# Optimization experiments

Measured on AMD Instinct MI355X. Metric: run time of the kernel, lower is better.

Reference implementation:

```python
import jax, jax.numpy as jnp
import numpy as np
from jax import lax

NEIGHBORS = 3


def _dwconv(x, w, b, dil):
    # depthwise Conv3d, kernel (9,3,3), temporal pad 4, spatial dilation `dil`
    out = lax.conv_general_dilated(
        x, w, window_strides=(1, 1, 1),
        padding=[(4, 4), (dil, dil), (dil, dil)],
        rhs_dilation=(1, dil, dil),
        dimension_numbers=('NCDHW', 'OIDHW', 'NCDHW'),
        feature_group_count=w.shape[0])
    return out + b[None, :, None, None, None]


def setup_inputs() -> dict:
    key = jax.random.key(0)
    ks = jax.random.split(key, 20)
    N, C, T, H, W = 2, 512, 96, 14, 14
    rc = C // 16
    nrm = lambda k, shape: (jax.random.normal(k, shape, jnp.float32) * 0.02)
    inp = {
        'x': jax.random.normal(ks[0], (N, C, T, H, W), jnp.float32),
        'down_conv2_w': nrm(ks[1], (C, C)),
        'down_conv_w': nrm(ks[2], (rc, C)),
        'conv_back_w': nrm(ks[3], (C, rc)),
        'weights2': jnp.ones((2 * NEIGHBORS,), jnp.float32) / (2 * NEIGHBORS),
        'weights4': jnp.ones((3,), jnp.float32) / 3,
        'weights': jnp.ones((3,), jnp.float32) / 3,
        'query': jax.random.uniform(ks[4], (1, 1, C), jnp.float32),
        'q_w': nrm(ks[5], (C, C)), 'q_b': nrm(ks[6], (C,)),
        'k_w': nrm(ks[7], (C, C)), 'k_b': nrm(ks[8], (C,)),
        'v_w': nrm(ks[9], (C, C)), 'v_b': nrm(ks[10], (C,)),
        'c_w': nrm(ks[11], (C, C)), 'c_b': nrm(ks[12], (C,)),
        'sa1_w': nrm(ks[13], (rc, 1, 9, 3, 3)), 'sa1_b': nrm(ks[14], (rc,)),
        'sa2_w': nrm(ks[15], (rc, 1, 9, 3, 3)), 'sa2_b': nrm(ks[16], (rc,)),
        'sa3_w': nrm(ks[17], (rc, 1, 9, 3, 3)), 'sa3_b': nrm(ks[18], (rc,)),
    }
    return inp


def reference(x, down_conv2_w, down_conv_w, conv_back_w, weights2, weights4, weights,
              query, q_w, q_b, k_w, k_b, v_w, v_b, c_w, c_b,
              sa1_w, sa1_b, sa2_w, sa2_b, sa3_w, sa3_b):
    N, C, T, H, W = x.shape
    nb = NEIGHBORS
    win = 2 * nb + 1

    # --- AttentionPool2d: single head, single learned query token ---
    kv = x.reshape(N, C, T, H * W).transpose(3, 0, 2, 1).reshape(H * W, N * T, C)  # (L,B,C)
    q = jnp.broadcast_to(query, (1, N * T, C))
    qp = (q @ q_w.T + q_b) * (C ** -0.5)          # head_dim == C since num_heads=1
    kp = kv @ k_w.T + k_b
    vp = kv @ v_w.T + v_b
    attn = jax.nn.softmax(jnp.einsum('pbc,lbc->bpl', qp, kp), axis=-1)  # (B,1,L)
    att_out = jnp.einsum('bpl,lbc->pbc', attn, vp) @ c_w.T + c_b        # (1,B,C)
    x_att = att_out.reshape(1, N, T, C).transpose(1, 3, 2, 0)           # (N,C,T,1)

    # --- pooled queries ---
    x_mean = jnp.mean(x, axis=(3, 4))[..., None]   # (N,C,T,1)
    x_max = jnp.max(x, axis=(3, 4))[..., None]     # (N,C,T,1)
    xq = x_mean * weights4[0] + x_max * weights4[1] + x_att * weights4[2]

    # --- 1x1 conv + temporal unfold (window 7, zero pad 3), drop center frame ---
    x2 = jnp.einsum('oc,ncthw->nothw', down_conv2_w, x)
    xp = jnp.pad(x2, ((0, 0), (0, 0), (nb, nb), (0, 0), (0, 0)))
    windows = jnp.stack([xp[:, :, i:i + T] for i in range(win)], axis=3)  # (N,C,T,7,H,W)
    idx = np.array([i for i in range(win) if i != nb])                    # exclude center
    upfold = windows[:, :, :, idx] * weights2[None, None, None, :, None, None]
    upfold = upfold.reshape(N, C, T, 2 * nb * H * W)                      # (N,C,T,L)

    # --- local correlation / clustering with sigmoid-0.5 gating ---
    aff = jnp.einsum('nctp,nctl->ntpl', xq, upfold)                       # (N,T,1,L)
    feat = jnp.einsum('nctl,ntpl->nctp', upfold, jax.nn.sigmoid(aff) - 0.5)  # (N,C,T,1)
    features = feat[..., None]                                            # (N,C,T,1,1)

    # --- multi-branch dilated depthwise conv fusion ---
    x_down = jnp.einsum('oc,ncthw->nothw', down_conv_w, x)                # (N,rc,T,H,W)
    agg = (_dwconv(x_down, sa1_w, sa1_b, 1) * weights[0]
           + _dwconv(x_down, sa2_w, sa2_b, 2) * weights[1]
           + _dwconv(x_down, sa3_w, sa3_b, 3) * weights[2])
    agg = jnp.einsum('oc,ncthw->nothw', conv_back_w, agg)                 # (N,C,T,H,W)

    return features * (jax.nn.sigmoid(agg) - 0.5)
```

## Files before the change

### kernel.cpp

```cpp
#include <hip/hip_runtime.h>
#include <hip/hip_bf16.h>

using bf16 = __hip_bfloat16;
typedef __attribute__((ext_vector_type(4))) unsigned short ushort4v;

#define N_  2
#define C_  512
#define T_  96
#define H_  14
#define W_  14
#define HW_ 196
#define RC_ 32
#define B_  (N_*T_)
#define SC_ (T_*HW_)
#define XTOT (N_*C_*T_*HW_)

#define VQB   0
#define VKB   512
#define VVB   1024
#define VCB   1536
#define VQRY  2048
#define VSAB  2560
#define VW2   2688
#define VW4   2696
#define VWTS  2700
#define VECS_TOTAL 2720

__device__ __forceinline__ float b2f(bf16 v){ return __bfloat162float(v); }
__device__ __forceinline__ float u2f(unsigned short u){ return __uint_as_float(((unsigned)u)<<16); }
__device__ __forceinline__ float sigm(float x){ return 1.f/(1.f+__expf(-x)); }
__device__ __forceinline__ unsigned short f2bu(float f){
    bf16 b = __float2bfloat16(f);
    return *(unsigned short*)&b;
}

__device__ __forceinline__ float ldd(const void* p, size_t i, bool f32){
    if (f32) return ((const float*)p)[i];
    else     return b2f(((const bf16*)p)[i]);
}

__global__ void probe_kernel(const void* __restrict__ x, int* __restrict__ flag){
    if (blockIdx.x==0 && threadIdx.x==0){
        const unsigned short* h = (const unsigned short*)x;
        int wild = 0;
        for (int i=0;i<128;i++){
            int e = (h[i] >> 7) & 0xFF;
            if (e < 100 || e > 150) wild++;
        }
        flag[0] = (wild > 16) ? 1 : 0;
    }
}

__global__ void prep_w2t_kernel(const void* __restrict__ dcw2, float* __restrict__ w2t,
                                const int* __restrict__ flag){
    bool f32 = flag[0]!=0;
    int i = blockIdx.x*256 + threadIdx.x;
    if (i < C_*C_){
        int in = i / C_, out = i % C_;
        w2t[i] = ldd(dcw2, (size_t)out*C_ + in, f32);
    }
}

#define PM_OLD (16384+16384+7776+512*5+96+6+3+3)
#define PM_TOTAL (PM_OLD + 262144 + 262144)
__global__ void prep_misc_kernel(const void* dcw, const void* cbw,
                                 const void* sa1w, const void* sa2w, const void* sa3w,
                                 const void* q_b, const void* k_b, const void* v_b,
                                 const void* c_b, const void* query,
                                 const void* sa1b, const void* sa2b, const void* sa3b,
                                 const void* w2, const void* w4, const void* wts,
                                 const void* v_w, const void* c_w,
                                 float* __restrict__ dwt, float* __restrict__ cbwf,
                                 float* __restrict__ saw, float* __restrict__ vecs,
                                 float* __restrict__ vwt, float* __restrict__ cwt,
                                 const int* __restrict__ flag){
    bool f32 = flag[0]!=0;
    int i = blockIdx.x*256 + threadIdx.x;
    if (i >= PM_TOTAL) return;
    if (i < 16384){ dwt[i] = ldd(dcw, i, f32); return; }
    i -= 16384;
    if (i < 16384){ cbwf[i] = ldd(cbw, i, f32); return; }
    i -= 16384;
    if (i < 7776){
        const void* s = (i<2592)? sa1w : ((i<5184)? sa2w : sa3w);
        int j = (i<2592)? i : ((i<5184)? i-2592 : i-5184);
        saw[i] = ldd(s, j, f32); return;
    }
    i -= 7776;
    if (i < 512){ vecs[VQB +i] = ldd(q_b,  i, f32); return; } i -= 512;
    if (i < 512){ vecs[VKB +i] = ldd(k_b,  i, f32); return; } i -= 512;
    if (i < 512){ vecs[VVB +i] = ldd(v_b,  i, f32); return; } i -= 512;
    if (i < 512){ vecs[VCB +i] = ldd(c_b,  i, f32); return; } i -= 512;
    if (i < 512){ vecs[VQRY+i] = ldd(query,i, f32); return; } i -= 512;
    if (i < 96){
        const void* s = (i<32)? sa1b : ((i<64)? sa2b : sa3b);
        vecs[VSAB+i] = ldd(s, i&31, f32); return;
    }
    i -= 96;
    if (i < 6){ vecs[VW2+i] = ldd(w2, i, f32); return; } i -= 6;
    if (i < 3){ vecs[VW4+i] = ldd(w4, i, f32); return; } i -= 3;
    if (i < 3){ vecs[VWTS+i] = ldd(wts, i, f32); return; } i -= 3;
    if (i < 262144){ int r=i/C_, c=i%C_; vwt[i] = ldd(v_w, (size_t)c*C_+r, f32); return; }
    i -= 262144;
    { int r=i/C_, c=i%C_; cwt[i] = ldd(c_w, (size_t)c*C_+r, f32); }
}

#define TCH 128
__global__ void __launch_bounds__(256) cvt_tr_kernel(const void* __restrict__ x,
                                                     bf16* __restrict__ xt,
                                                     const int* __restrict__ flag){
    bool f32 = flag[0]!=0;
    int bt = blockIdx.x;
    int n = bt / T_, t = bt % T_;
    int c0 = blockIdx.y * TCH;
    __shared__ bf16 tile[TCH*197];
    int tid = threadIdx.x;
    const size_t ibase = (((size_t)n*C_ + c0)*T_ + t)*HW_;
    for (int i=tid; i<TCH*49; i+=256){
        int cr = i / 49, l4 = (i - cr*49)*4;
        size_t gi = ibase + (size_t)cr*SC_ + l4;
        bf16* dp = &tile[cr*197 + l4];
        if (f32){
            float4 v = *(const float4*)((const float*)x + gi);
            dp[0]=__float2bfloat16(v.x); dp[1]=__float2bfloat16(v.y);
            dp[2]=__float2bfloat16(v.z); dp[3]=__float2bfloat16(v.w);
        } else {
            ushort4v u = *(const ushort4v*)((const bf16*)x + gi);
            #pragma unroll
            for (int k=0;k<4;k++) *(unsigned short*)&dp[k] = u[k];
        }
    }
    __syncthreads();
    bf16* obase = xt + (size_t)bt*HW_*C_ + c0;
    for (int i=tid; i<HW_*TCH/4; i+=256){
        int l = i >> 5, cg = (i & 31)*4;
        ushort4v u;
        #pragma unroll
        for (int k=0;k<4;k++) u[k] = *(unsigned short*)&tile[(cg+k)*197 + l];
        *(ushort4v*)(obase + (size_t)l*C_ + cg) = u;
    }
}

__global__ void __launch_bounds__(64) qproj1_kernel(const void* __restrict__ q_w,
        const float* __restrict__ vecs, float* __restrict__ qp,
        const int* __restrict__ flag){
    bool f32 = flag[0]!=0;
    int c = blockIdx.x;
    int lane = threadIdx.x;
    float acc = 0.f;
    #pragma unroll
    for (int i=lane;i<C_;i+=64)
        acc += vecs[VQRY+i] * ldd(q_w, (size_t)c*C_+i, f32);
    #pragma unroll
    for (int off=32; off>0; off>>=1) acc += __shfl_down(acc, off);
    if (lane==0) qp[c] = (acc + vecs[VQB+c]) * 0.044194173824159216f;
}

__global__ void __launch_bounds__(256) qproj2_kernel(const void* __restrict__ k_w,
        const float* __restrict__ vecs, const float* __restrict__ qp,
        float* __restrict__ qk_out, const int* __restrict__ flag){
    bool f32 = flag[0]!=0;
    __shared__ float sh[256];
    int tid = threadIdx.x;
    if (blockIdx.x < 8){
        int c = blockIdx.x*64 + (tid&63);
        int isub = tid>>6;
        float acc = 0.f;
        for (int i=isub*128; i<isub*128+128; i++)
            acc += qp[i] * ldd(k_w, (size_t)i*C_ + c, f32);
        sh[tid] = acc;
        __syncthreads();
        if (tid < 64)
            qk_out[c] = sh[tid] + sh[tid+64] + sh[tid+128] + sh[tid+192];
    } else {
        float acc = 0.f;
        for (int i=tid;i<C_;i+=256) acc += qp[i]*vecs[VKB+i];
        sh[tid] = acc;
        __syncthreads();
        if (tid==0){
            float d=0.f;
            for (int i=0;i<256;i++) d += sh[i];
            qk_out[C_] = d;
        }
    }
}

__global__ void __launch_bounds__(512) f1_kernel(const bf16* __restrict__ xt,
        const float* __restrict__ qk, const float* __restrict__ vecs,
        float* __restrict__ pooled, float* __restrict__ mm){
    int b = blockIdx.x;
    __shared__ float sm[HW_];
    __shared__ float red[2];
    __shared__ float r8[8][C_];
    int tid = threadIdx.x, wave = tid>>6, lane = tid&63;
    float qkr[8];
    #pragma unroll
    for (int k=0;k<4;k++){ qkr[k] = qk[lane*4+k]; qkr[4+k] = qk[256+lane*4+k]; }
    float qkC = qk[C_];
    const bf16* fbase = xt + (size_t)b*HW_*C_;
    for (int l=wave; l<HW_; l+=8){
        const bf16* row = fbase + (size_t)l*C_;
        ushort4v u1 = *(const ushort4v*)(row + lane*4);
        ushort4v u2 = *(const ushort4v*)(row + 256 + lane*4);
        float a = 0.f;
        #pragma unroll
        for (int k=0;k<4;k++) a += qkr[k]*u2f(u1[k]) + qkr[4+k]*u2f(u2[k]);
        #pragma unroll
        for (int off=32; off>0; off>>=1) a += __shfl_down(a, off);
        if (lane==0) sm[l] = a + qkC;
    }
    __syncthreads();
    if (tid < 64){
        float m = -1e30f;
        for (int l=tid; l<HW_; l+=64) m = fmaxf(m, sm[l]);
        #pragma unroll
        for (int off=32; off>0; off>>=1) m = fmaxf(m, __shfl_down(m, off));
        if (tid==0) red[0] = m;
    }
    __syncthreads();
    if (tid < HW_) sm[tid] = __expf(sm[tid]-red[0]);
    __syncthreads();
    if (tid < 64){
        float s = 0.f;
        for (int l=tid; l<HW_; l+=64) s += sm[l];
        #pragma unroll
        for (int off=32; off>0; off>>=1) s += __shfl_down(s, off);
        if (tid==0) red[1] = 1.f/s;
    }
    __syncthreads();
    if (tid < HW_) sm[tid] *= red[1];
    __syncthreads();
    float sa[8], pa[8], ma[8];
    #pragma unroll
    for (int k=0;k<8;k++){ sa[k]=0.f; pa[k]=0.f; ma[k]=-1e30f; }
    for (int l=wave; l<HW_; l+=8){
        const bf16* row = fbase + (size_t)l*C_;
        ushort4v u1 = *(const ushort4v*)(row + lane*4);
        ushort4v u2 = *(const ushort4v*)(row + 256 + lane*4);
        float smv = sm[l];
        #pragma unroll
        for (int k=0;k<4;k++){
            float v1 = u2f(u1[k]), v2 = u2f(u2[k]);
            sa[k]   += v1; ma[k]   = fmaxf(ma[k],  v1); pa[k]   += smv*v1;
            sa[4+k] += v2; ma[4+k] = fmaxf(ma[4+k],v2); pa[4+k] += smv*v2;
        }
    }
    int c1 = lane*4, c2 = 256+lane*4;
    #pragma unroll
    for (int k=0;k<4;k++){ r8[wave][c1+k]=pa[k]; r8[wave][c2+k]=pa[4+k]; }
    __syncthreads();
    int c = tid;
    float pltot = 0.f;
    #pragma unroll
    for (int w=0;w<8;w++) pltot += r8[w][c];
    __syncthreads();
    #pragma unroll
    for (int k=0;k<4;k++){ r8[wave][c1+k]=sa[k]; r8[wave][c2+k]=sa[4+k]; }
    __syncthreads();
    float stot = 0.f;
    #pragma unroll
    for (int w=0;w<8;w++) stot += r8[w][c];
    __syncthreads();
    #pragma unroll
    for (int k=0;k<4;k++){ r8[wave][c1+k]=ma[k]; r8[wave][c2+k]=ma[4+k]; }
    __syncthreads();
    float mtot = -1e30f;
    #pragma unroll
    for (int w=0;w<8;w++) mtot = fmaxf(mtot, r8[w][c]);
    pooled[(size_t)b*C_+c] = pltot;
    float w40=vecs[VW4+0], w41=vecs[VW4+1];
    mm[(size_t)b*C_+c] = stot*(1.f/HW_)*w40 + mtot*w41;
}

__global__ void __launch_bounds__(512) proj_kernel(const float* __restrict__ pooled,
        const float* __restrict__ mm, const float* __restrict__ vwt,
        const float* __restrict__ cwt, const void* __restrict__ dcw2,
        const float* __restrict__ vecs, float* __restrict__ xq,
        float* __restrict__ yq, const int* __restrict__ flag){
    bool f32 = flag[0]!=0;
    int b = blockIdx.x, c = threadIdx.x;
    __shared__ float p_s[C_];
    __shared__ float pre_s[C_];
    __shared__ float xq_s[C_];
    p_s[c] = pooled[(size_t)b*C_ + c];
    __syncthreads();
    float pre = vecs[VVB+c];
    for (int i=0;i<C_;i++) pre += p_s[i]*vwt[(size_t)i*C_+c];
    pre_s[c] = pre;
    __syncthreads();
    float att = vecs[VCB+c];
    for (int i=0;i<C_;i++) att += pre_s[i]*cwt[(size_t)i*C_+c];
    float xqv = mm[(size_t)b*C_+c] + vecs[VW4+2]*att;
    xq[(size_t)b*C_+c] = xqv;
    xq_s[c] = xqv;
    __syncthreads();
    float yqv = 0.f;
    for (int i=0;i<C_;i++) yqv += xq_s[i]*ldd(dcw2, (size_t)i*C_+c, f32);
    yq[(size_t)b*C_+c] = yqv;
}

#define QROWS 49
#define B6C   (B_*6*C_)
__global__ void __launch_bounds__(512) corr2gz_kernel(const bf16* __restrict__ xt,
        const float* __restrict__ yq, const float* __restrict__ vecs,
        float* __restrict__ zpart){
    const int offs[6] = {-3,-2,-1,1,2,3};
    int frame = blockIdx.x;
    int qq = blockIdx.y;
    int n = frame / T_, tp = frame % T_;
    int l0 = qq*QROWS;
    __shared__ bf16 xs[QROWS*C_];
    __shared__ float a_s[6][QROWS];
    int tid = threadIdx.x, lane = tid&63, wave = tid>>6;
    const ushort4v* src = (const ushort4v*)(xt + ((size_t)frame*HW_ + l0)*C_);
    ushort4v* dst = (ushort4v*)xs;
    for (int i=tid; i<QROWS*C_/4; i+=512) dst[i] = src[i];
    bool val[6]; float w2r[6]; float yqr[6][8];
    #pragma unroll
    for (int jj=0;jj<6;jj++){
        int tt = tp - offs[jj];
        val[jj] = (tt>=0 && tt<T_);
        w2r[jj] = vecs[VW2+jj];
        if (val[jj]){
            const float* yb = yq + (size_t)(n*T_+tt)*C_;
            #pragma unroll
            for (int k=0;k<4;k++){ yqr[jj][k]=yb[lane*4+k]; yqr[jj][4+k]=yb[256+lane*4+k]; }
        } else {
            #pragma unroll
            for (int k=0;k<8;k++) yqr[jj][k]=0.f;
        }
    }
    __syncthreads();
    for (int li=wave; li<QROWS; li+=8){
        ushort4v u1 = *(const ushort4v*)(xs + li*C_ + lane*4);
        ushort4v u2 = *(const ushort4v*)(xs + li*C_ + 256 + lane*4);
        float xf[8];
        #pragma unroll
        for (int k=0;k<4;k++){ xf[k]=u2f(u1[k]); xf[4+k]=u2f(u2[k]); }
        float a[6];
        #pragma unroll
        for (int jj=0;jj<6;jj++){
            float s=0.f;
            #pragma unroll
            for (int k=0;k<8;k++) s += yqr[jj][k]*xf[k];
            a[jj]=s;
        }
        #pragma unroll
        for (int off=32; off>0; off>>=1){
            #pragma unroll
            for (int jj=0;jj<6;jj++) a[jj] += __shfl_down(a[jj], off);
        }
        if (lane==0){
            #pragma unroll
            for (int jj=0;jj<6;jj++)
                a_s[jj][li] = val[jj] ? w2r[jj]*(sigm(w2r[jj]*a[jj])-0.5f) : 0.f;
        }
    }
    __syncthreads();
    int e = tid;
    float acc[6] = {0.f,0.f,0.f,0.f,0.f,0.f};
    for (int li=0; li<QROWS; ++li){
        float xv = b2f(xs[li*C_ + e]);
        #pragma unroll
        for (int jj=0;jj<6;jj++) acc[jj] += a_s[jj][li]*xv;
    }
    #pragma unroll
    for (int jj=0;jj<6;jj++){
        if (val[jj]){
            int b = n*T_ + (tp - offs[jj]);
            zpart[(size_t)qq*B6C + ((size_t)b*6+jj)*C_ + e] = acc[jj];
        }
    }
}

__global__ void __launch_bounds__(128) corr2f_kernel(const float* __restrict__ zpart,
        const float* __restrict__ w2t, float* __restrict__ feat){
    const int offs[6] = {-3,-2,-1,1,2,3};
    int b = blockIdx.x, c0 = blockIdx.y*128;
    int t = b % T_;
    int tid = threadIdx.x;
    __shared__ float z_s[C_];
    for (int e=tid; e<C_; e+=128){
        float s = 0.f;
        #pragma unroll
        for (int jj=0;jj<6;jj++){
            int tj = t + offs[jj];
            if (tj<0 || tj>=T_) continue;
            const float* zp = zpart + ((size_t)b*6+jj)*C_ + e;
            s += zp[0] + zp[B6C] + zp[2*B6C] + zp[3*(size_t)B6C];
        }
        z_s[e] = s;
    }
    __syncthreads();
    int c = c0 + tid;
    float acc = 0.f;
    for (int e=0;e<C_;e++) acc += w2t[(size_t)e*C_+c]*z_s[e];
    feat[(size_t)b*C_+c] = acc;
}

#define XPAD 8
#define XROW (C_+XPAD)
__global__ void __launch_bounds__(256) xdown_kernel(const bf16* __restrict__ xt,
                                                    const float* __restrict__ dwt,
                                                    bf16* __restrict__ xd){
    int b = blockIdx.x, n=b/T_, t=b%T_;
    int l0 = blockIdx.y*8;
    int nl = HW_ - l0; if (nl > 8) nl = 8;
    __shared__ bf16 xs[8*XROW];
    int tid = threadIdx.x;
    const bf16* fbase = xt + (size_t)b*HW_*C_ + (size_t)l0*C_;
    for (int i=tid; i<nl*(C_/4); i+=256){
        int row = i >> 7, gc = (i & 127)*4;
        *(ushort4v*)(xs + row*XROW + gc) = *(const ushort4v*)(fbase + (size_t)row*C_ + gc);
    }
    __syncthreads();
    int r = tid>>3, ls = tid&7;
    if (ls < nl){
        float acc = 0.f;
        const bf16* xr = xs + ls*XROW;
        const float* wr = dwt + (size_t)r*C_;
        #pragma unroll 4
        for (int c4=0; c4<C_; c4+=4){
            ushort4v u = *(const ushort4v*)(xr + c4);
            float4 w = *(const float4*)(wr + c4);
            acc += w.x*u2f(u[0]) + w.y*u2f(u[1])
                 + w.z*u2f(u[2]) + w.w*u2f(u[3]);
        }
        xd[(((size_t)n*RC_+r)*T_ + t)*HW_ + l0 + ls] = __float2bfloat16(acc);
    }
}

#define TPAD 21
#define TROW 20
#define TFRM (TROW*TPAD)
__global__ void __launch_bounds__(256) dwconv_kernel(const bf16* __restrict__ xd,
        const float* __restrict__ saw, const float* __restrict__ vecs,
        float* __restrict__ aggs){
    int nr = blockIdx.x;
    int t  = blockIdx.y;
    int r  = nr % RC_;
    __shared__ float tile[9*TFRM];
    __shared__ float wsm[3][81];
    int tid = threadIdx.x;
    for (int i=tid;i<9*TFRM;i+=256) tile[i] = 0.f;
    if (tid < 81){
        wsm[0][tid]=saw[       r*81+tid];
        wsm[1][tid]=saw[2592 + r*81+tid];
        wsm[2][tid]=saw[5184 + r*81+tid];
    }
    __syncthreads();
    const bf16* base = xd + (size_t)nr*T_*HW_;
    for (int i=tid;i<9*HW_;i+=256){
        int kt = i/HW_, hw = i - kt*HW_;
        int tg = t - 4 + kt;
        if (tg>=0 && tg<T_){
            int h = hw/W_, w = hw - h*W_;
            tile[kt*TFRM + (h+3)*TPAD + (w+3)] = b2f(base[(size_t)tg*HW_ + hw]);
        }
    }
    __syncthreads();
    if (tid < HW_){
        int h = tid/W_, w = tid - h*W_;
        float w0=vecs[VWTS+0], w1=vecs[VWTS+1], w2v=vecs[VWTS+2];
        float cbias = w0*vecs[VSAB+r] + w1*vecs[VSAB+32+r] + w2v*vecs[VSAB+64+r];
        float bacc[3];
        #pragma unroll
        for (int br=0;br<3;br++){
            int d = br+1;
            float s = 0.f;
            #pragma unroll
            for (int kt=0;kt<9;kt++){
                const float* tb = &tile[kt*TFRM + (h+3-d)*TPAD + (w+3-d)];
                const float* wp = &wsm[br][kt*9];
                s += wp[0]*tb[0]          + wp[1]*tb[d]          + wp[2]*tb[2*d]
                   + wp[3]*tb[d*TPAD]     + wp[4]*tb[d*TPAD+d]   + wp[5]*tb[d*TPAD+2*d]
                   + wp[6]*tb[2*d*TPAD]   + wp[7]*tb[2*d*TPAD+d] + wp[8]*tb[2*d*TPAD+2*d];
            }
            bacc[br] = s;
        }
        float acc = cbias + w0*bacc[0] + w1*bacc[1] + w2v*bacc[2];
        aggs[(size_t)nr*T_*HW_ + (size_t)t*HW_ + tid] = acc;
    }
}

__global__ void __launch_bounds__(256) final_kernel(const float* __restrict__ aggs,
                                                    const float* __restrict__ cbwf,
                                                    const float* __restrict__ feat,
                                                    float* __restrict__ out){
    int b = blockIdx.x, n = b/T_, t = b%T_;
    int c0 = blockIdx.y*128;
    int hw = threadIdx.x;
    if (hw >= HW_) return;
    float ra[RC_];
    #pragma unroll
    for (int r=0;r<RC_;r++)
        ra[r] = aggs[(((size_t)n*RC_+r)*T_ + t)*HW_ + hw];
    const float* fb = feat + (size_t)b*C_;
    for (int ci=0;ci<128;ci++){
        int c = c0+ci;
        const float* wr = cbwf + c*RC_;
        float a = 0.f;
        #pragma unroll
        for (int r=0;r<RC_;r++) a += wr[r]*ra[r];
        out[(((size_t)n*C_+c)*T_ + t)*HW_ + hw] = fb[c]*(sigm(a)-0.5f);
    }
}

extern "C" void kernel_launch(void* const* d_in, const int* in_sizes, int n_in,
                              void* d_out, int out_size, void* d_ws, size_t ws_size,
                              hipStream_t stream){
    const void* x      = d_in[0];
    const void* dcw2   = d_in[1];
    const void* dcw    = d_in[2];
    const void* cbw    = d_in[3];
    const void* w2     = d_in[4];
    const void* w4     = d_in[5];
    const void* wts    = d_in[6];
    const void* query  = d_in[7];
    const void* q_w    = d_in[8];
    const void* q_b    = d_in[9];
    const void* k_w    = d_in[10];
    const void* k_b    = d_in[11];
    const void* v_w    = d_in[12];
    const void* v_b    = d_in[13];
    const void* c_w    = d_in[14];
    const void* c_b    = d_in[15];
    const void* sa1w   = d_in[16];
    const void* sa1b   = d_in[17];
    const void* sa2w   = d_in[18];
    const void* sa2b   = d_in[19];
    const void* sa3w   = d_in[20];
    const void* sa3b   = d_in[21];
    float* out = (float*)d_out;

    float* ws    = (float*)d_ws;
    int*   flag  = (int*)ws;
    float* qk    = ws + 16;
    float* qp    = qk + 1024;
    float* pooled= qp + 1024;
    float* mm    = pooled + 98304;
    float* xq    = mm + 98304;
    float* yq    = xq + 98304;
    float* feat  = yq + 98304;
    float* w2t   = feat + 98304;
    float* vwt   = w2t + 262144;
    float* cwt   = vwt + 262144;
    float* dwt   = cwt + 262144;
    float* cbwf  = dwt + 16384;
    float* saw   = cbwf + 16384;
    float* vecs  = saw + 7936;
    float* aggs  = vecs + VECS_TOTAL;
    bf16*  xd    = (bf16*)(aggs + 1204224);
    bf16*  xt    = (bf16*)d_out;
    float* zpart = (float*)(xt + (size_t)XTOT);

    probe_kernel<<<1, 64, 0, stream>>>(x, flag);
    prep_w2t_kernel<<<(C_*C_+255)/256, 256, 0, stream>>>(dcw2, w2t, flag);
    prep_misc_kernel<<<(PM_TOTAL+255)/256, 256, 0, stream>>>(
        dcw, cbw, sa1w, sa2w, sa3w, q_b, k_b, v_b, c_b, query,
        sa1b, sa2b, sa3b, w2, w4, wts, v_w, c_w,
        dwt, cbwf, saw, vecs, vwt, cwt, flag);
    cvt_tr_kernel<<<dim3(B_, C_/TCH), 256, 0, stream>>>(x, xt, flag);

    qproj1_kernel<<<C_, 64, 0, stream>>>(q_w, vecs, qp, flag);
    qproj2_kernel<<<9, 256, 0, stream>>>(k_w, vecs, qp, qk, flag);
    f1_kernel<<<B_, 512, 0, stream>>>(xt, qk, vecs, pooled, mm);
    proj_kernel<<<B_, C_, 0, stream>>>(pooled, mm, vwt, cwt, dcw2, vecs, xq, yq, flag);

    corr2gz_kernel<<<dim3(B_, 4), 512, 0, stream>>>(xt, yq, vecs, zpart);
    corr2f_kernel<<<dim3(B_, 4), 128, 0, stream>>>(zpart, w2t, feat);

    xdown_kernel<<<dim3(B_, 25), 256, 0, stream>>>(xt, dwt, xd);
    dwconv_kernel<<<dim3(N_*RC_, T_), 256, 0, stream>>>(xd, saw, vecs, aggs);
    final_kernel<<<dim3(B_, 4), 256, 0, stream>>>(aggs, cbwf, feat, out);
}
```

Measured before the change: 647.1 us.

## Fuse channel down-projection into correlation kernel reusing its shared-memory tile

The separate xdown kernel, which re-read the whole bf16 transposed input from global memory, is removed. Its 512-to-32 channel projection is now computed inside corr2gz_kernel from the 49-row tile already staged in shared memory, with each wave producing four output channels. The shared tile rows are padded to 516 elements to reduce LDS bank conflicts on the row-strided reads. This saves one full pass over the input and one launch, but adds serial work to each correlation block, which could lengthen its critical path given the small grid of 768 blocks.

```diff
diff --git a/kernel.cpp b/kernel.cpp
--- a/kernel.cpp
+++ b/kernel.cpp
@@ -300,21 +300,25 @@
 }
 
 #define QROWS 49
+#define XR    516
 #define B6C   (B_*6*C_)
 __global__ void __launch_bounds__(512) corr2gz_kernel(const bf16* __restrict__ xt,
         const float* __restrict__ yq, const float* __restrict__ vecs,
-        float* __restrict__ zpart){
+        const float* __restrict__ dwt, float* __restrict__ zpart,
+        bf16* __restrict__ xd){
     const int offs[6] = {-3,-2,-1,1,2,3};
     int frame = blockIdx.x;
     int qq = blockIdx.y;
     int n = frame / T_, tp = frame % T_;
     int l0 = qq*QROWS;
-    __shared__ bf16 xs[QROWS*C_];
+    __shared__ bf16 xs[QROWS*XR];
     __shared__ float a_s[6][QROWS];
     int tid = threadIdx.x, lane = tid&63, wave = tid>>6;
     const ushort4v* src = (const ushort4v*)(xt + ((size_t)frame*HW_ + l0)*C_);
-    ushort4v* dst = (ushort4v*)xs;
-    for (int i=tid; i<QROWS*C_/4; i+=512) dst[i] = src[i];
+    for (int i=tid; i<QROWS*128; i+=512){
+        int row = i>>7, g4 = (i&127)*4;
+        *(ushort4v*)(xs + row*XR + g4) = src[i];
+    }
     bool val[6]; float w2r[6]; float yqr[6][8];
     #pragma unroll
     for (int jj=0;jj<6;jj++){
@@ -332,8 +336,8 @@
     }
     __syncthreads();
     for (int li=wave; li<QROWS; li+=8){
-        ushort4v u1 = *(const ushort4v*)(xs + li*C_ + lane*4);
-        ushort4v u2 = *(const ushort4v*)(xs + li*C_ + 256 + lane*4);
+        ushort4v u1 = *(const ushort4v*)(xs + li*XR + lane*4);
+        ushort4v u2 = *(const ushort4v*)(xs + li*XR + 256 + lane*4);
         float xf[8];
         #pragma unroll
         for (int k=0;k<4;k++){ xf[k]=u2f(u1[k]); xf[4+k]=u2f(u2[k]); }
@@ -357,18 +361,50 @@
         }
     }
     __syncthreads();
-    int e = tid;
-    float acc[6] = {0.f,0.f,0.f,0.f,0.f,0.f};
-    for (int li=0; li<QROWS; ++li){
-        float xv = b2f(xs[li*C_ + e]);
-        #pragma unroll
-        for (int jj=0;jj<6;jj++) acc[jj] += a_s[jj][li]*xv;
-    }
-    #pragma unroll
-    for (int jj=0;jj<6;jj++){
-        if (val[jj]){
-            int b = n*T_ + (tp - offs[jj]);
-            zpart[(size_t)qq*B6C + ((size_t)b*6+jj)*C_ + e] = acc[jj];
+    {
+        int e = tid;
+        float acc[6] = {0.f,0.f,0.f,0.f,0.f,0.f};
+        for (int li=0; li<QROWS; ++li){
+            float xv = b2f(xs[li*XR + e]);
+            #pragma unroll
+            for (int jj=0;jj<6;jj++) acc[jj] += a_s[jj][li]*xv;
+        }
+        #pragma unroll
+        for (int jj=0;jj<6;jj++){
+            if (val[jj]){
+                int b = n*T_ + (tp - offs[jj]);
+                zpart[(size_t)qq*B6C + ((size_t)b*6+jj)*C_ + e] = acc[jj];
+            }
+        }
+    }
+    {
+        int r0 = __builtin_amdgcn_readfirstlane(wave)*4;
+        if (lane < QROWS){
+            const bf16* xr = xs + lane*XR;
+            const float* w0 = dwt + (size_t)(r0+0)*C_;
+            const float* w1 = dwt + (size_t)(r0+1)*C_;
+            const float* w2p= dwt + (size_t)(r0+2)*C_;
+            const float* w3 = dwt + (size_t)(r0+3)*C_;
+            float a0=0.f, a1=0.f, a2=0.f, a3=0.f;
+            for (int c4=0; c4<C_; c4+=4){
+                ushort4v u = *(const ushort4v*)(xr + c4);
+                float x0=u2f(u[0]), x1=u2f(u[1]), x2=u2f(u[2]), x3=u2f(u[3]);
+                float4 wa = *(const float4*)(w0 + c4);
+                float4 wb = *(const float4*)(w1 + c4);
+                float4 wc = *(const float4*)(w2p+ c4);
+                float4 wd = *(const float4*)(w3 + c4);
+                a0 += wa.x*x0 + wa.y*x1 + wa.z*x2 + wa.w*x3;
+                a1 += wb.x*x0 + wb.y*x1 + wb.z*x2 + wb.w*x3;
+                a2 += wc.x*x0 + wc.y*x1 + wc.z*x2 + wc.w*x3;
+                a3 += wd.x*x0 + wd.y*x1 + wd.z*x2 + wd.w*x3;
+            }
+            int gl = l0 + lane;
+            size_t base = (((size_t)n*RC_ + r0)*T_ + tp)*HW_ + gl;
+            size_t step = (size_t)T_*HW_;
+            xd[base       ] = __float2bfloat16(a0);
+            xd[base+  step] = __float2bfloat16(a1);
+            xd[base+2*step] = __float2bfloat16(a2);
+            xd[base+3*step] = __float2bfloat16(a3);
         }
     }
 }
@@ -396,38 +432,6 @@
     float acc = 0.f;
     for (int e=0;e<C_;e++) acc += w2t[(size_t)e*C_+c]*z_s[e];
     feat[(size_t)b*C_+c] = acc;
-}
-
-#define XPAD 8
-#define XROW (C_+XPAD)
-__global__ void __launch_bounds__(256) xdown_kernel(const bf16* __restrict__ xt,
-                                                    const float* __restrict__ dwt,
-                                                    bf16* __restrict__ xd){
-    int b = blockIdx.x, n=b/T_, t=b%T_;
-    int l0 = blockIdx.y*8;
-    int nl = HW_ - l0; if (nl > 8) nl = 8;
-    __shared__ bf16 xs[8*XROW];
-    int tid = threadIdx.x;
-    const bf16* fbase = xt + (size_t)b*HW_*C_ + (size_t)l0*C_;
-    for (int i=tid; i<nl*(C_/4); i+=256){
-        int row = i >> 7, gc = (i & 127)*4;
-        *(ushort4v*)(xs + row*XROW + gc) = *(const ushort4v*)(fbase + (size_t)row*C_ + gc);
-    }
-    __syncthreads();
-    int r = tid>>3, ls = tid&7;
-    if (ls < nl){
-        float acc = 0.f;
-        const bf16* xr = xs + ls*XROW;
-        const float* wr = dwt + (size_t)r*C_;
-        #pragma unroll 4
-        for (int c4=0; c4<C_; c4+=4){
-            ushort4v u = *(const ushort4v*)(xr + c4);
-            float4 w = *(const float4*)(wr + c4);
-            acc += w.x*u2f(u[0]) + w.y*u2f(u[1])
-                 + w.z*u2f(u[2]) + w.w*u2f(u[3]);
-        }
-        xd[(((size_t)n*RC_+r)*T_ + t)*HW_ + l0 + ls] = __float2bfloat16(acc);
-    }
 }
 
 #define TPAD 21
@@ -567,10 +571,9 @@
     f1_kernel<<<B_, 512, 0, stream>>>(xt, qk, vecs, pooled, mm);
     proj_kernel<<<B_, C_, 0, stream>>>(pooled, mm, vwt, cwt, dcw2, vecs, xq, yq, flag);
 
-    corr2gz_kernel<<<dim3(B_, 4), 512, 0, stream>>>(xt, yq, vecs, zpart);
+    corr2gz_kernel<<<dim3(B_, 4), 512, 0, stream>>>(xt, yq, vecs, dwt, zpart, xd);
     corr2f_kernel<<<dim3(B_, 4), 128, 0, stream>>>(zpart, w2t, feat);
 
-    xdown_kernel<<<dim3(B_, 25), 256, 0, stream>>>(xt, dwt, xd);
     dwconv_kernel<<<dim3(N_*RC_, T_), 256, 0, stream>>>(xd, saw, vecs, aggs);
     final_kernel<<<dim3(B_, 4), 256, 0, stream>>>(aggs, cbwf, feat, out);
 }
```

After: 637.9 us. No clear change (-1.4%).
